# Kernel tuning notes

Hardware: AMD Instinct MI355X
Metric: run time of the kernel (lower is better)

Reference implementation:

```python
import jax, jax.numpy as jnp
import numpy as np

B, CIN, COUT = 64, 192, 384
WS = 7            # window size (kernel_size)
NH = 12           # num heads
HD = COUT // NH   # head dim = 32
HID = 4 * COUT    # mlp hidden (mlp_ratio=4)
NB = 2            # num R2L blocks
EPS = 1e-5        # torch LayerNorm default

def _ln(x, g, b):
    m = jnp.mean(x, -1, keepdims=True)
    v = jnp.mean((x - m) ** 2, -1, keepdims=True)
    return (x - m) * jax.lax.rsqrt(v + EPS) * g + b

def _gelu(x):
    return jax.nn.gelu(x, approximate=False)  # torch nn.GELU (exact erf)

def _rel_index():
    # replicates AttentionWithRelPos index: tmp[qx-kx+ws-1, qy-ky+ws-1]
    r = np.arange(WS * WS)
    qr, qc = r // WS, r % WS
    return jnp.asarray((qr[:, None] - qr[None, :] + WS - 1) * (2 * WS - 1)
                       + (qc[:, None] - qc[None, :] + WS - 1))

REL_IDX = _rel_index()  # [49, 49]

def _attn(x, qkv_w, qkv_b, pw, pb, rel_pos, patch_attn):
    Bw, N, C = x.shape
    qkv = (x @ qkv_w + qkv_b).reshape(Bw, N, 3, NH, HD).transpose(2, 0, 3, 1, 4)
    q, k, v = qkv[0], qkv[1], qkv[2]
    attn = jnp.einsum('bhqd,bhkd->bhqk', q, k) * (HD ** -0.5)
    if patch_attn:
        # rel-pos bias only over patch-patch entries; cls row/col get 0
        bias = jnp.pad(rel_pos[:, REL_IDX], ((0, 0), (1, 0), (1, 0)))
        attn = attn + bias[None]
    attn = jax.nn.softmax(attn, -1)
    out = jnp.einsum('bhqk,bhkd->bhqd', attn, v).transpose(0, 2, 1, 3).reshape(Bw, N, C)
    return out @ pw + pb

def _proj(x, g, b, cw, cb):
    # LayerNorm2d + GELU + depthwise-grouped stride-2 conv (ks=3, pad=1)
    y = _gelu(_ln(x.transpose(0, 2, 3, 1), g, b))
    y = jax.lax.conv_general_dilated(y, cw, (2, 2), ((1, 1), (1, 1)),
                                     feature_group_count=CIN,
                                     dimension_numbers=('NHWC', 'HWIO', 'NHWC')) + cb
    return y.transpose(0, 3, 1, 2)

def reference(cls_tokens, patch_tokens, proj_ln_g, proj_ln_b, proj_conv_w, proj_conv_b,
              n0_g, n0_b, n1_g, n1_b, n2_g, n2_b, qkv_w, qkv_b, ap_w, ap_b,
              rel_pos, fc1_w, fc1_b, fc2_w, fc2_b):
    # Projection (shared weights for cls and patch streams)
    c = _proj(cls_tokens, proj_ln_g, proj_ln_b, proj_conv_w, proj_conv_b)   # [B,C,4,4]
    p = _proj(patch_tokens, proj_ln_g, proj_ln_b, proj_conv_w, proj_conv_b) # [B,C,28,28]
    Bi, C, Hk, Wk = c.shape
    kh, kw = p.shape[2] // Hk, p.shape[3] // Wk  # = (7,7); divisible -> mask=None path
    # convert_to_flatten_layout: unfold into non-overlapping kh*kw windows,
    # window grid row-major, tokens within window row-major, cls token prepended
    pt = p.reshape(Bi, C, Hk, kh, Wk, kw).transpose(0, 2, 4, 3, 5, 1)
    pt = pt.reshape(Bi * Hk * Wk, kh * kw, C)
    ct = c.reshape(Bi, C, Hk * Wk).transpose(0, 2, 1).reshape(Bi * Hk * Wk, 1, C)
    out = jnp.concatenate([ct, pt], 1)  # [B*nwin, 1+49, C]
    nwin = Hk * Wk
    for i in range(NB):
        # regional (cls) attention across windows of the same image
        cls_t = out[:, :1].reshape(Bi, nwin, C)
        cls_t = cls_t + _attn(_ln(cls_t, n0_g[i], n0_b[i]), qkv_w[i], qkv_b[i],
                              ap_w[i], ap_b[i], rel_pos[i], False)
        out = jnp.concatenate([cls_t.reshape(-1, 1, C), out[:, 1:]], 1)
        # local (regional-to-local) attention within each window with rel-pos bias
        out = out + _attn(_ln(out, n1_g[i], n1_b[i]), qkv_w[i], qkv_b[i],
                          ap_w[i], ap_b[i], rel_pos[i], True)
        # MLP (expand is None since input_channels == output_channels)
        h = _gelu(_ln(out, n2_g[i], n2_b[i]) @ fc1_w[i] + fc1_b[i])
        out = out + h @ fc2_w[i] + fc2_b[i]
    # convert_to_spatial_layout (fold)
    cls_out = out[:, 0].reshape(Bi, Hk, Wk, C).transpose(0, 3, 1, 2)
    patch_out = out[:, 1:].reshape(Bi, Hk, Wk, kh, kw, C)
    patch_out = patch_out.transpose(0, 5, 1, 3, 2, 4).reshape(Bi, C, Hk * kh, Wk * kw)
    return cls_out, patch_out

def setup_inputs():
    key = jax.random.key(0)
    ks = jax.random.split(key, 8)
    std = 0.02
    return dict(
        cls_tokens=jax.random.normal(ks[0], (B, CIN, 8, 8), jnp.float32),
        patch_tokens=jax.random.normal(ks[1], (B, CIN, 56, 56), jnp.float32),
        proj_ln_g=jnp.ones((CIN,), jnp.float32),
        proj_ln_b=jnp.zeros((CIN,), jnp.float32),
        proj_conv_w=jax.random.normal(ks[2], (3, 3, 1, COUT), jnp.float32) * std,
        proj_conv_b=jnp.zeros((COUT,), jnp.float32),
        n0_g=jnp.ones((NB, COUT), jnp.float32),
        n0_b=jnp.zeros((NB, COUT), jnp.float32),
        n1_g=jnp.ones((NB, COUT), jnp.float32),
        n1_b=jnp.zeros((NB, COUT), jnp.float32),
        n2_g=jnp.ones((NB, COUT), jnp.float32),
        n2_b=jnp.zeros((NB, COUT), jnp.float32),
        qkv_w=jax.random.normal(ks[3], (NB, COUT, 3 * COUT), jnp.float32) * std,
        qkv_b=jnp.zeros((NB, 3 * COUT), jnp.float32),
        ap_w=jax.random.normal(ks[4], (NB, COUT, COUT), jnp.float32) * std,
        ap_b=jnp.zeros((NB, COUT), jnp.float32),
        rel_pos=jax.random.normal(ks[5], (NB, NH, (2 * WS - 1) ** 2), jnp.float32) * std,
        fc1_w=jax.random.normal(ks[6], (NB, COUT, HID), jnp.float32) * std,
        fc1_b=jnp.zeros((NB, HID), jnp.float32),
        fc2_w=jax.random.normal(ks[7], (NB, HID, COUT), jnp.float32) * std,
        fc2_b=jnp.zeros((NB, COUT), jnp.float32),
    )
```

## Files before the change

kernel.cpp:

```cpp
#include <hip/hip_runtime.h>
#include <hip/hip_bf16.h>
#include <math.h>


typedef __attribute__((ext_vector_type(8))) short short8;
typedef __attribute__((ext_vector_type(4))) float f32x4;

__device__ __forceinline__ float gelu_f(float x) {
  return 0.5f * x * (1.0f + erff(x * 0.70710678118654752440f));
}

__global__ __launch_bounds__(256) void k_ln_gelu_c192(
    const float* __restrict__ x, float* __restrict__ t,
    const float* __restrict__ g, const float* __restrict__ b,
    int HW, int npos)
{
  int wid = threadIdx.x >> 6, lane = threadIdx.x & 63;
  int pos = blockIdx.x * 4 + wid;
  if (pos >= npos) return;
  int bi = pos / HW, p = pos - bi * HW;
  const float* xp = x + (long)bi * 192 * HW + p;
  float v0 = xp[(long)(lane      ) * HW];
  float v1 = xp[(long)(lane +  64) * HW];
  float v2 = xp[(long)(lane + 128) * HW];
  float s  = v0 + v1 + v2;
  float sq = v0*v0 + v1*v1 + v2*v2;
  #pragma unroll
  for (int o = 1; o < 64; o <<= 1) { s += __shfl_xor(s, o); sq += __shfl_xor(sq, o); }
  float mean = s * (1.0f/192.0f);
  float var  = sq * (1.0f/192.0f) - mean*mean;
  float rstd = rsqrtf(var + 1e-5f);
  float* tp = t + (long)pos * 192;
  int c0 = lane, c1 = lane + 64, c2 = lane + 128;
  tp[c0] = gelu_f((v0-mean)*rstd*g[c0] + b[c0]);
  tp[c1] = gelu_f((v1-mean)*rstd*g[c1] + b[c1]);
  tp[c2] = gelu_f((v2-mean)*rstd*g[c2] + b[c2]);
}

__global__ __launch_bounds__(384) void k_dwconv(
    const float* __restrict__ t, const float* __restrict__ w,
    const float* __restrict__ bias, float* __restrict__ XT,
    int Hin, int Win, int Hout, int Wout, int isCls)
{
  int o = threadIdx.x;
  int blk = blockIdx.x;
  int b = blk / Hout, oh = blk - b * Hout;
  int ic = o >> 1;
  float wr[9];
  #pragma unroll
  for (int q = 0; q < 9; ++q) wr[q] = w[q * 384 + o];
  float bo = bias[o];
  const float* tb = t + (long)b * Hin * Win * 192;
  for (int ow = 0; ow < Wout; ++ow) {
    float acc = bo;
    #pragma unroll
    for (int ky = 0; ky < 3; ++ky) {
      int ih = 2*oh - 1 + ky;
      if (ih < 0 || ih >= Hin) continue;
      #pragma unroll
      for (int kx = 0; kx < 3; ++kx) {
        int iw = 2*ow - 1 + kx;
        if (iw < 0 || iw >= Win) continue;
        acc += wr[ky*3+kx] * tb[((long)ih * Win + iw) * 192 + ic];
      }
    }
    int row;
    if (isCls) row = (b * 16 + oh * Wout + ow) * 50;
    else       row = (b * 16 + (oh/7)*4 + (ow/7)) * 50 + 1 + (oh%7)*7 + (ow%7);
    XT[(long)row * 384 + o] = acc;
  }
}

__global__ __launch_bounds__(256) void k_ln384(
    const float* __restrict__ in, long istride,
    __hip_bfloat16* __restrict__ out, long ostride,
    const float* __restrict__ g, const float* __restrict__ b, int rows)
{
  int wid = threadIdx.x >> 6, lane = threadIdx.x & 63;
  int r = blockIdx.x * 4 + wid;
  if (r >= rows) return;
  const float* ip = in + (long)r * istride;
  float x[6]; float s = 0.f, sq = 0.f;
  #pragma unroll
  for (int j = 0; j < 6; ++j) {
    x[j] = ip[lane + 64*j];
    s += x[j]; sq += x[j]*x[j];
  }
  #pragma unroll
  for (int o = 1; o < 64; o <<= 1) { s += __shfl_xor(s, o); sq += __shfl_xor(sq, o); }
  float mean = s * (1.0f/384.0f);
  float var  = sq * (1.0f/384.0f) - mean*mean;
  float rstd = rsqrtf(var + 1e-5f);
  __hip_bfloat16* op = out + (long)r * ostride;
  #pragma unroll
  for (int j = 0; j < 6; ++j) {
    int c = lane + 64*j;
    op[c] = __float2bfloat16((x[j]-mean)*rstd*g[c] + b[c]);
  }
}

__global__ __launch_bounds__(256) void k_wT(
    const float* __restrict__ W, __hip_bfloat16* __restrict__ Wt, int K, int N)
{
  __shared__ ushort t[64][65];
  int n0 = blockIdx.x * 64, k0 = blockIdx.y * 64;
  int c = threadIdx.x & 63, r4 = threadIdx.x >> 6;
  #pragma unroll
  for (int s = 0; s < 16; ++s) {
    int k = r4 + s*4;
    __hip_bfloat16 h = __float2bfloat16(W[(long)(k0+k)*N + n0 + c]);
    t[k][c] = *(ushort*)&h;
  }
  __syncthreads();
  #pragma unroll
  for (int s = 0; s < 16; ++s) {
    int n = r4 + s*4;
    ushort u = t[c][n];
    Wt[(long)(n0+n)*K + k0 + c] = *(__hip_bfloat16*)&u;
  }
}

__global__ __launch_bounds__(256) void k_gemm_bf16(
    const ushort* __restrict__ A, const ushort* __restrict__ Bt,
    const float* __restrict__ bias, void* __restrict__ Cv,
    int K, int lda, int ldbt, int ldc, int flags)
{
  __shared__ ushort As[128*32];
  __shared__ ushort Bs[128*32];
  int tid = threadIdx.x;
  int w = tid >> 6, lane = tid & 63;
  int m0 = blockIdx.y * 128, n0 = blockIdx.x * 128;
  int wr = (w >> 1) * 64, wc = (w & 1) * 64;
  f32x4 acc[4][4] = {};

  int sRow = lane >> 2;
  int sCol = (lane & 3) * 8;
  const ushort* Abase = A  + (long)m0 * lda + sCol;
  const ushort* Bbase = Bt + (long)n0 * ldbt + sCol;

  for (int k0 = 0; k0 < K; k0 += 32) {
    #pragma unroll
    for (int p = 0; p < 2; ++p) {
      int chunk = w + 4*p;
      int row = chunk * 16 + sRow;
      __builtin_amdgcn_global_load_lds(
        (const __attribute__((address_space(1))) void*)(Abase + (long)row*lda + k0),
        (__attribute__((address_space(3))) void*)(As + chunk*512), 16, 0, 0);
      __builtin_amdgcn_global_load_lds(
        (const __attribute__((address_space(1))) void*)(Bbase + (long)row*ldbt + k0),
        (__attribute__((address_space(3))) void*)(Bs + chunk*512), 16, 0, 0);
    }
    __syncthreads();

    short8 af[4], bf[4];
    int kq = (lane >> 4) * 8;
    int fr = lane & 15;
    #pragma unroll
    for (int mi = 0; mi < 4; ++mi)
      af[mi] = *(const short8*)(As + (wr + mi*16 + fr)*32 + kq);
    #pragma unroll
    for (int ni = 0; ni < 4; ++ni)
      bf[ni] = *(const short8*)(Bs + (wc + ni*16 + fr)*32 + kq);
    #pragma unroll
    for (int mi = 0; mi < 4; ++mi)
      #pragma unroll
      for (int ni = 0; ni < 4; ++ni)
        acc[mi][ni] = __builtin_amdgcn_mfma_f32_16x16x32_bf16(af[mi], bf[ni], acc[mi][ni], 0, 0, 0);
    __syncthreads();
  }

  int colq = lane & 15, rowq = (lane >> 4) * 4;
  #pragma unroll
  for (int mi = 0; mi < 4; ++mi) {
    #pragma unroll
    for (int ni = 0; ni < 4; ++ni) {
      int col = n0 + wc + ni*16 + colq;
      float bv = bias[col];
      #pragma unroll
      for (int r = 0; r < 4; ++r) {
        int m = m0 + wr + mi*16 + rowq + r;
        float v = acc[mi][ni][r] + bv;
        if (flags & 2) v = gelu_f(v);
        if (flags & 4) {
          ((__hip_bfloat16*)Cv)[(long)m*ldc + col] = __float2bfloat16(v);
        } else {
          float* Cp = (float*)Cv + (long)m*ldc + col;
          float o = v;
          if (flags & 1) o += *Cp;
          *Cp = o;
        }
      }
    }
  }
}

__global__ __launch_bounds__(256) void k_attn2(
    const float* __restrict__ qkv, __hip_bfloat16* __restrict__ o,
    const float* __restrict__ relpos, int N, int ld, int ldo)
{
  int g = blockIdx.x / 12, h = blockIdx.x % 12;
  __shared__ float q[50][36];
  __shared__ float kv[50][36];
  __shared__ float S[50][52];
  __shared__ float rsum[64];
  int tid = threadIdx.x;
  int row0 = g * N;
  const float* base = qkv + (long)row0 * ld + h * 32;

  for (int e = tid; e < N * 32; e += 256) {
    int i = e >> 5, d = e & 31;
    long off = (long)i * ld + d;
    q[i][d]  = base[off];
    kv[i][d] = base[off + 384];
  }
  __syncthreads();

  const float scale = 0.17677669529663687f;
  const float* rph = relpos ? relpos + h * 169 : (const float*)0;
  for (int e = tid; e < N * N; e += 256) {
    int i = e / N, j = e - i * N;
    const float4* qp = (const float4*)q[i];
    const float4* kp = (const float4*)kv[j];
    float ax = 0.f, ay = 0.f, az = 0.f, aw = 0.f;
    #pragma unroll
    for (int d4 = 0; d4 < 8; ++d4) {
      float4 a = qp[d4], b = kp[d4];
      ax += a.x*b.x; ay += a.y*b.y; az += a.z*b.z; aw += a.w*b.w;
    }
    float acc = ((ax+ay)+(az+aw)) * scale;
    if (rph && i > 0 && j > 0) {
      int qi = i - 1, ki = j - 1;
      int qr = qi / 7, qc = qi - qr * 7;
      int kr = ki / 7, kc = ki - kr * 7;
      acc += rph[(qr - kr + 6) * 13 + (qc - kc + 6)];
    }
    S[i][j] = acc;
  }
  __syncthreads();

  for (int e = tid; e < N * 32; e += 256) {
    int i = e >> 5, d = e & 31;
    kv[i][d] = base[(long)i * ld + d + 768];
  }
  int wid = tid >> 6, lane = tid & 63;
  for (int r = wid; r < N; r += 4) {
    float v = (lane < N) ? S[r][lane] : -1e30f;
    float m = v;
    #pragma unroll
    for (int o2 = 32; o2 > 0; o2 >>= 1) m = fmaxf(m, __shfl_xor(m, o2));
    float e = (lane < N) ? __expf(v - m) : 0.f;
    float s = e;
    #pragma unroll
    for (int o2 = 32; o2 > 0; o2 >>= 1) s += __shfl_xor(s, o2);
    if (lane < N) S[r][lane] = e;
    if (lane == 0) rsum[r] = 1.0f / s;
  }
  __syncthreads();

  for (int u = tid; u < N * 8; u += 256) {
    int i = u >> 3, d4 = u & 7;
    float ax = 0.f, ay = 0.f, az = 0.f, aw = 0.f;
    for (int j = 0; j < N; ++j) {
      float p = S[i][j];
      float4 vv = *(const float4*)&kv[j][d4*4];
      ax += p*vv.x; ay += p*vv.y; az += p*vv.z; aw += p*vv.w;
    }
    float rs = rsum[i];
    __hip_bfloat16* op = o + (long)(row0 + i) * ldo + h*32 + d4*4;
    op[0] = __float2bfloat16(ax * rs);
    op[1] = __float2bfloat16(ay * rs);
    op[2] = __float2bfloat16(az * rs);
    op[3] = __float2bfloat16(aw * rs);
  }
}

__global__ __launch_bounds__(256) void k_fold(
    const float* __restrict__ XT, float* __restrict__ out)
{
  long idx = (long)blockIdx.x * 256 + threadIdx.x;
  if (idx < 393216) {
    int b = (int)(idx / (384*16));
    int rem = (int)(idx % (384*16));
    int c = rem / 16, p = rem % 16;
    out[idx] = XT[((long)(b*16 + p) * 50) * 384 + c];
  } else {
    long j = idx - 393216;
    int b = (int)(j / (384*784));
    int rem = (int)(j % (384*784));
    int c = rem / 784, p = rem % 784;
    int oh = p / 28, ow = p % 28;
    int row = (b*16 + (oh/7)*4 + ow/7) * 50 + 1 + (oh%7)*7 + (ow%7);
    out[idx] = XT[(long)row * 384 + c];
  }
}

extern "C" void kernel_launch(void* const* d_in, const int* in_sizes, int n_in,
                              void* d_out, int out_size, void* d_ws, size_t ws_size,
                              hipStream_t stream)
{
  const float* cls_in   = (const float*)d_in[0];
  const float* patch_in = (const float*)d_in[1];
  const float* pg   = (const float*)d_in[2];
  const float* pb   = (const float*)d_in[3];
  const float* cw   = (const float*)d_in[4];
  const float* cb   = (const float*)d_in[5];
  const float* n0g  = (const float*)d_in[6];
  const float* n0b  = (const float*)d_in[7];
  const float* n1g  = (const float*)d_in[8];
  const float* n1b  = (const float*)d_in[9];
  const float* n2g  = (const float*)d_in[10];
  const float* n2b  = (const float*)d_in[11];
  const float* qkvw = (const float*)d_in[12];
  const float* qkvb = (const float*)d_in[13];
  const float* apw  = (const float*)d_in[14];
  const float* apb  = (const float*)d_in[15];
  const float* rp   = (const float*)d_in[16];
  const float* f1w  = (const float*)d_in[17];
  const float* f1b  = (const float*)d_in[18];
  const float* f2w  = (const float*)d_in[19];
  const float* f2b  = (const float*)d_in[20];
  float* out = (float*)d_out;

  float*          XT = (float*)d_ws;
  __hip_bfloat16* LN = (__hip_bfloat16*)(XT + 19660800);
  float*          SC = (float*)((char*)LN + 39321600);
  __hip_bfloat16* OB = (__hip_bfloat16*)(SC + 58982400);
  __hip_bfloat16* WT = (__hip_bfloat16*)((char*)OB + 39321600);
  float* tP = SC;
  float* tC = SC + 38535168;

  k_ln_gelu_c192<<<50176, 256, 0, stream>>>(patch_in, tP, pg, pb, 3136, 200704);
  k_ln_gelu_c192<<<1024,  256, 0, stream>>>(cls_in,   tC, pg, pb, 64,   4096);
  k_dwconv<<<1792, 384, 0, stream>>>(tP, cw, cb, XT, 56, 56, 28, 28, 0);
  k_dwconv<<<256,  384, 0, stream>>>(tC, cw, cb, XT, 8, 8, 4, 4, 1);

  for (int i = 0; i < 2; ++i) {
    __hip_bfloat16* wb = WT + (long)i * 1769472;
    k_wT<<<dim3(18,6),  256, 0, stream>>>(qkvw + (long)i*442368, wb,           384, 1152);
    k_wT<<<dim3(6,6),   256, 0, stream>>>(apw  + (long)i*147456, wb + 442368,  384, 384);
    k_wT<<<dim3(24,6),  256, 0, stream>>>(f1w  + (long)i*589824, wb + 589824,  384, 1536);
    k_wT<<<dim3(6,24),  256, 0, stream>>>(f2w  + (long)i*589824, wb + 1179648, 1536, 384);
  }

  for (int i = 0; i < 2; ++i) {
    __hip_bfloat16* wb = WT + (long)i * 1769472;
    const ushort* qwT  = (const ushort*)(wb);
    const ushort* apT  = (const ushort*)(wb + 442368);
    const ushort* f1T  = (const ushort*)(wb + 589824);
    const ushort* f2T  = (const ushort*)(wb + 1179648);
    const float* qb  = qkvb + i*1152;
    const float* ab  = apb  + i*384;
    const float* rpi = rp   + (long)i*12*169;

    k_ln384<<<256, 256, 0, stream>>>(XT, 19200, LN, 384, n0g + i*384, n0b + i*384, 1024);
    k_gemm_bf16<<<dim3(9,8), 256, 0, stream>>>((const ushort*)LN, qwT, qb, SC, 384, 384, 384, 1152, 0);
    k_attn2<<<768, 256, 0, stream>>>(SC, OB, (const float*)0, 16, 1152, 384);
    k_gemm_bf16<<<dim3(3,8), 256, 0, stream>>>((const ushort*)OB, apT, ab, XT, 384, 384, 384, 19200, 1);

    k_ln384<<<12800, 256, 0, stream>>>(XT, 384, LN, 384, n1g + i*384, n1b + i*384, 51200);
    k_gemm_bf16<<<dim3(9,400), 256, 0, stream>>>((const ushort*)LN, qwT, qb, SC, 384, 384, 384, 1152, 0);
    k_attn2<<<12288, 256, 0, stream>>>(SC, OB, rpi, 50, 1152, 384);
    k_gemm_bf16<<<dim3(3,400), 256, 0, stream>>>((const ushort*)OB, apT, ab, XT, 384, 384, 384, 384, 1);

    k_ln384<<<12800, 256, 0, stream>>>(XT, 384, LN, 384, n2g + i*384, n2b + i*384, 51200);
    k_gemm_bf16<<<dim3(12,400), 256, 0, stream>>>((const ushort*)LN, f1T, f1b + i*1536,
                                                  SC, 384, 384, 384, 1536, 2|4);
    k_gemm_bf16<<<dim3(3,400), 256, 0, stream>>>((const ushort*)SC, f2T, f2b + i*384,
                                                 XT, 1536, 1536, 1536, 384, 1);
  }

  k_fold<<<76800, 256, 0, stream>>>(XT, out);
}
```

Measured before the change: 2.447 ms.

## Rewrite window attention with bf16 MFMA, one head per wave, bf16 QKV

Replaces the scalar fp32 attention kernel with a templated MFMA version. Each wave handles one head of a window, computes QK^T and PV with 16x16x32 bf16 MFMA, and does the softmax in registers, writing bf16 probabilities to LDS. The QKV GEMMs now emit bf16 instead of fp32, which halves the intermediate traffic. The cost is lower precision in the scores and probabilities, plus padding of 50 tokens up to 64.

Result: faster. 2.235 ms (-8.7%).

```diff
diff --git a/kernel.cpp b/kernel.cpp
--- a/kernel.cpp
+++ b/kernel.cpp
@@ -194,83 +194,161 @@
   }
 }
 
-__global__ __launch_bounds__(256) void k_attn2(
-    const float* __restrict__ qkv, __hip_bfloat16* __restrict__ o,
+template<int NT>
+__global__ __launch_bounds__(256) void k_attn3(
+    const ushort* __restrict__ qkv, __hip_bfloat16* __restrict__ o,
     const float* __restrict__ relpos, int N, int ld, int ldo)
 {
-  int g = blockIdx.x / 12, h = blockIdx.x % 12;
-  __shared__ float q[50][36];
-  __shared__ float kv[50][36];
-  __shared__ float S[50][52];
-  __shared__ float rsum[64];
+  constexpr int NP   = NT * 16;
+  constexpr int KTOK = (NP < 32) ? 32 : NP;
+  constexpr int KS   = 40;
+  constexpr int PS   = KTOK + 8;
+  constexpr int QP_ELE = NP * PS;
+  constexpr int K_ELE  = NP * KS;
+  constexpr int VT_ELE = 32 * PS;
+  constexpr int W_ELE  = QP_ELE + K_ELE + VT_ELE;
+
+  __shared__ __align__(16) ushort lds[4 * W_ELE];
+  __shared__ float rpl[4][172];
+
   int tid = threadIdx.x;
+  int w = tid >> 6, lane = tid & 63;
+  int head = blockIdx.y * 4 + w;
+  int g = blockIdx.x;
   int row0 = g * N;
-  const float* base = qkv + (long)row0 * ld + h * 32;
-
-  for (int e = tid; e < N * 32; e += 256) {
+  const ushort* base = qkv + (long)row0 * ld + head * 32;
+
+  ushort* Ql = lds + w * W_ELE;
+  ushort* Kl = Ql + QP_ELE;
+  ushort* Vt = Kl + K_ELE;
+
+  for (int e = lane; e < NP * 16; e += 64) {
+    int i = e >> 4, c = e & 15;
+    uint qv = 0, kv = 0;
+    if (i < N) {
+      const uint* p = (const uint*)(base + (long)i * ld);
+      qv = p[c];
+      kv = p[c + 192];
+    }
+    *(uint*)(Ql + i * KS + c * 2) = qv;
+    *(uint*)(Kl + i * KS + c * 2) = kv;
+  }
+  for (int e = lane; e < NP * 32; e += 64) {
     int i = e >> 5, d = e & 31;
-    long off = (long)i * ld + d;
-    q[i][d]  = base[off];
-    kv[i][d] = base[off + 384];
-  }
-  __syncthreads();
+    ushort vv = 0;
+    if (i < N) vv = base[(long)i * ld + 768 + d];
+    Vt[d * PS + i] = vv;
+  }
+  if constexpr (KTOK > NP) {
+    for (int e = lane; e < 32 * (KTOK - NP); e += 64) {
+      int d = e / (KTOK - NP), i = NP + e % (KTOK - NP);
+      Vt[d * PS + i] = 0;
+    }
+  }
+  if constexpr (NT == 4) {
+    for (int e = lane; e < 169; e += 64) rpl[w][e] = relpos[head * 169 + e];
+  }
+  asm volatile("s_waitcnt lgkmcnt(0)" ::: "memory");
+  __builtin_amdgcn_sched_barrier(0);
+
+  int fr = lane & 15, kq = (lane >> 4) * 8;
+  short8 qf[NT], kf[NT];
+  #pragma unroll
+  for (int mi = 0; mi < NT; ++mi)
+    qf[mi] = *(const short8*)(Ql + (mi*16 + fr) * KS + kq);
+  #pragma unroll
+  for (int ni = 0; ni < NT; ++ni)
+    kf[ni] = *(const short8*)(Kl + (ni*16 + fr) * KS + kq);
+  f32x4 s[NT][NT] = {};
+  #pragma unroll
+  for (int mi = 0; mi < NT; ++mi)
+    #pragma unroll
+    for (int ni = 0; ni < NT; ++ni)
+      s[mi][ni] = __builtin_amdgcn_mfma_f32_16x16x32_bf16(qf[mi], kf[ni], s[mi][ni], 0, 0, 0);
 
   const float scale = 0.17677669529663687f;
-  const float* rph = relpos ? relpos + h * 169 : (const float*)0;
-  for (int e = tid; e < N * N; e += 256) {
-    int i = e / N, j = e - i * N;
-    const float4* qp = (const float4*)q[i];
-    const float4* kp = (const float4*)kv[j];
-    float ax = 0.f, ay = 0.f, az = 0.f, aw = 0.f;
-    #pragma unroll
-    for (int d4 = 0; d4 < 8; ++d4) {
-      float4 a = qp[d4], b = kp[d4];
-      ax += a.x*b.x; ay += a.y*b.y; az += a.z*b.z; aw += a.w*b.w;
-    }
-    float acc = ((ax+ay)+(az+aw)) * scale;
-    if (rph && i > 0 && j > 0) {
-      int qi = i - 1, ki = j - 1;
-      int qr = qi / 7, qc = qi - qr * 7;
-      int kr = ki / 7, kc = ki - kr * 7;
-      acc += rph[(qr - kr + 6) * 13 + (qc - kc + 6)];
-    }
-    S[i][j] = acc;
-  }
-  __syncthreads();
-
-  for (int e = tid; e < N * 32; e += 256) {
-    int i = e >> 5, d = e & 31;
-    kv[i][d] = base[(long)i * ld + d + 768];
-  }
-  int wid = tid >> 6, lane = tid & 63;
-  for (int r = wid; r < N; r += 4) {
-    float v = (lane < N) ? S[r][lane] : -1e30f;
-    float m = v;
-    #pragma unroll
-    for (int o2 = 32; o2 > 0; o2 >>= 1) m = fmaxf(m, __shfl_xor(m, o2));
-    float e = (lane < N) ? __expf(v - m) : 0.f;
-    float s = e;
-    #pragma unroll
-    for (int o2 = 32; o2 > 0; o2 >>= 1) s += __shfl_xor(s, o2);
-    if (lane < N) S[r][lane] = e;
-    if (lane == 0) rsum[r] = 1.0f / s;
-  }
-  __syncthreads();
-
-  for (int u = tid; u < N * 8; u += 256) {
-    int i = u >> 3, d4 = u & 7;
-    float ax = 0.f, ay = 0.f, az = 0.f, aw = 0.f;
-    for (int j = 0; j < N; ++j) {
-      float p = S[i][j];
-      float4 vv = *(const float4*)&kv[j][d4*4];
-      ax += p*vv.x; ay += p*vv.y; az += p*vv.z; aw += p*vv.w;
-    }
-    float rs = rsum[i];
-    __hip_bfloat16* op = o + (long)(row0 + i) * ldo + h*32 + d4*4;
-    op[0] = __float2bfloat16(ax * rs);
-    op[1] = __float2bfloat16(ay * rs);
-    op[2] = __float2bfloat16(az * rs);
-    op[3] = __float2bfloat16(aw * rs);
+  int colq = lane & 15, rowq = (lane >> 4) * 4;
+  int jv[NT], kr[NT], kc[NT];
+  #pragma unroll
+  for (int ni = 0; ni < NT; ++ni) {
+    jv[ni] = ni*16 + colq;
+    int kd = jv[ni] - 1;
+    kr[ni] = kd / 7; kc[ni] = kd - kr[ni]*7;
+  }
+  #pragma unroll
+  for (int mi = 0; mi < NT; ++mi) {
+    #pragma unroll
+    for (int r = 0; r < 4; ++r) {
+      int i = mi*16 + rowq + r;
+      float m = -1e30f;
+      float sv[NT];
+      if constexpr (NT == 4) {
+        int qd = i - 1;
+        int qr = qd / 7, qc = qd - qr*7;
+        #pragma unroll
+        for (int ni = 0; ni < NT; ++ni) {
+          float v = s[mi][ni][r] * scale;
+          if (i > 0 && i < N && jv[ni] > 0 && jv[ni] < N)
+            v += rpl[w][(qr - kr[ni] + 6)*13 + (qc - kc[ni] + 6)];
+          if (jv[ni] >= N) v = -1e30f;
+          sv[ni] = v; m = fmaxf(m, v);
+        }
+      } else {
+        #pragma unroll
+        for (int ni = 0; ni < NT; ++ni) { sv[ni] = s[mi][ni][r] * scale; m = fmaxf(m, sv[ni]); }
+      }
+      #pragma unroll
+      for (int o2 = 1; o2 < 16; o2 <<= 1) m = fmaxf(m, __shfl_xor(m, o2));
+      float sum = 0.f;
+      #pragma unroll
+      for (int ni = 0; ni < NT; ++ni) { sv[ni] = __expf(sv[ni] - m); sum += sv[ni]; }
+      #pragma unroll
+      for (int o2 = 1; o2 < 16; o2 <<= 1) sum += __shfl_xor(sum, o2);
+      float rs = 1.0f / sum;
+      #pragma unroll
+      for (int ni = 0; ni < NT; ++ni) {
+        __hip_bfloat16 h = __float2bfloat16(sv[ni] * rs);
+        Ql[i * PS + jv[ni]] = *(ushort*)&h;
+      }
+    }
+  }
+  if constexpr (KTOK > NP) {
+    for (int e = lane; e < NP * (KTOK - NP); e += 64) {
+      int i = e >> 4, j = NP + (e & 15);
+      Ql[i * PS + j] = 0;
+    }
+  }
+  asm volatile("s_waitcnt lgkmcnt(0)" ::: "memory");
+  __builtin_amdgcn_sched_barrier(0);
+
+  f32x4 oacc[NT][2] = {};
+  #pragma unroll
+  for (int ks = 0; ks < KTOK / 32; ++ks) {
+    short8 pf[NT];
+    #pragma unroll
+    for (int mi = 0; mi < NT; ++mi)
+      pf[mi] = *(const short8*)(Ql + (mi*16 + fr) * PS + ks*32 + kq);
+    #pragma unroll
+    for (int di = 0; di < 2; ++di) {
+      short8 vf = *(const short8*)(Vt + (di*16 + fr) * PS + ks*32 + kq);
+      #pragma unroll
+      for (int mi = 0; mi < NT; ++mi)
+        oacc[mi][di] = __builtin_amdgcn_mfma_f32_16x16x32_bf16(pf[mi], vf, oacc[mi][di], 0, 0, 0);
+    }
+  }
+
+  #pragma unroll
+  for (int mi = 0; mi < NT; ++mi) {
+    #pragma unroll
+    for (int r = 0; r < 4; ++r) {
+      int i = mi*16 + rowq + r;
+      if (i < N) {
+        __hip_bfloat16* op = o + (long)(row0 + i) * ldo + head * 32;
+        #pragma unroll
+        for (int di = 0; di < 2; ++di)
+          op[di*16 + colq] = __float2bfloat16(oacc[mi][di][r]);
+      }
+    }
   }
 }
 
@@ -353,13 +431,13 @@
     const float* rpi = rp   + (long)i*12*169;
 
     k_ln384<<<256, 256, 0, stream>>>(XT, 19200, LN, 384, n0g + i*384, n0b + i*384, 1024);
-    k_gemm_bf16<<<dim3(9,8), 256, 0, stream>>>((const ushort*)LN, qwT, qb, SC, 384, 384, 384, 1152, 0);
-    k_attn2<<<768, 256, 0, stream>>>(SC, OB, (const float*)0, 16, 1152, 384);
+    k_gemm_bf16<<<dim3(9,8), 256, 0, stream>>>((const ushort*)LN, qwT, qb, SC, 384, 384, 384, 1152, 4);
+    k_attn3<1><<<dim3(64,3), 256, 0, stream>>>((const ushort*)SC, OB, (const float*)0, 16, 1152, 384);
     k_gemm_bf16<<<dim3(3,8), 256, 0, stream>>>((const ushort*)OB, apT, ab, XT, 384, 384, 384, 19200, 1);
 
     k_ln384<<<12800, 256, 0, stream>>>(XT, 384, LN, 384, n1g + i*384, n1b + i*384, 51200);
-    k_gemm_bf16<<<dim3(9,400), 256, 0, stream>>>((const ushort*)LN, qwT, qb, SC, 384, 384, 384, 1152, 0);
-    k_attn2<<<12288, 256, 0, stream>>>(SC, OB, rpi, 50, 1152, 384);
+    k_gemm_bf16<<<dim3(9,400), 256, 0, stream>>>((const ushort*)LN, qwT, qb, SC, 384, 384, 384, 1152, 4);
+    k_attn3<4><<<dim3(1024,3), 256, 0, stream>>>((const ushort*)SC, OB, rpi, 50, 1152, 384);
     k_gemm_bf16<<<dim3(3,400), 256, 0, stream>>>((const ushort*)OB, apT, ab, XT, 384, 384, 384, 384, 1);
 
     k_ln384<<<12800, 256, 0, stream>>>(XT, 384, LN, 384, n2g + i*384, n2b + i*384, 51200);
```
